# Optimization experiments

Hardware: AMD Instinct MI355X
Metric: run time of the kernel (lower is better)

The kernel has to match this reference:

```python
import jax, jax.numpy as jnp
import numpy as np

LABEL_SMOOTHING = 0.1
K_SLOPE = 5.0
N, D = 8192, 256


def setup_inputs() -> dict:
    key = jax.random.key(0)
    k1, k2, k3 = jax.random.split(key, 3)
    return {
        "image_features1": jax.random.normal(k1, (N, D), dtype=jnp.float32),
        "image_features2": jax.random.normal(k2, (N, D), dtype=jnp.float32),
        "logit_scale": jnp.asarray(14.2857, dtype=jnp.float32),  # ~ 1/0.07 CLIP temp
        "positive_weights": jax.random.normal(k3, (N,), dtype=jnp.float32),
    }


def _l2_normalize(x, axis=-1, eps=1e-12):
    # matches F.normalize(dim=-1)
    norm = jnp.linalg.norm(x, axis=axis, keepdims=True)
    return x / jnp.maximum(norm, eps)


def _weighted_infonce(sim, eps):
    # per row i: (1-eps_i)*(-sim[i,i] + lse_i) + eps_i*(-mean(sim[i,:]) + lse_i)
    #          = lse_i - (1-eps_i)*sim[i,i] - eps_i*mean_i
    n = sim.shape[0]
    lse = jax.nn.logsumexp(sim, axis=1)            # [n]
    diag = jnp.diagonal(sim)                       # [n]
    row_mean = jnp.mean(sim, axis=1)               # [n]
    per_row = lse - (1.0 - eps) * diag - eps * row_mean
    return jnp.sum(per_row) / n


def reference(image_features1, image_features2, logit_scale, positive_weights):
    f1 = _l2_normalize(image_features1)
    f2 = _l2_normalize(image_features2)
    logits12 = logit_scale * (f1 @ f2.T)           # [N, N]
    # eps = 1 - (1 - label_smoothing) * sigmoid(k * w)
    eps = 1.0 - (1.0 - LABEL_SMOOTHING) * jax.nn.sigmoid(K_SLOPE * positive_weights)
    loss1 = _weighted_infonce(logits12, eps)
    loss2 = _weighted_infonce(logits12.T, eps)
    return (loss1 + loss2) / 2.0
```

## Files before the change

kernel.cpp:

```cpp
#include <hip/hip_runtime.h>
#include <hip/hip_bf16.h>

#define NN 8192
#define DD 256
#define LOG2E 1.4426950408889634f
#define LN2f 0.6931471805599453f

typedef __attribute__((ext_vector_type(8))) short short8;
typedef __attribute__((ext_vector_type(4))) float f32x4;

__device__ __forceinline__ unsigned short f2bf(float x) {
    unsigned int u = __float_as_uint(x);
    u += 0x7fff + ((u >> 16) & 1);
    return (unsigned short)(u >> 16);
}
__device__ __forceinline__ float epsf(float w) {
    return 1.f - 0.9f / (1.f + __expf(-5.f * w));
}

__global__ __launch_bounds__(256) void nrm_kernel(
    const float* __restrict__ f1, const float* __restrict__ f2,
    const float* __restrict__ scale_p, const float* __restrict__ wts,
    unsigned short* __restrict__ f1n, unsigned short* __restrict__ f2n,
    float* __restrict__ diag, float* __restrict__ rse, float* __restrict__ cse,
    float* __restrict__ S1p, float* __restrict__ S2p,
    float* __restrict__ T1p, float* __restrict__ T2p)
{
    __shared__ float4 red[4][256];
    const int w = threadIdx.x >> 6, lane = threadIdx.x & 63;
    const int row = blockIdx.x * 4 + w;
    const float4 a = reinterpret_cast<const float4*>(f1 + (size_t)row * DD)[lane];
    const float4 b = reinterpret_cast<const float4*>(f2 + (size_t)row * DD)[lane];
    float sa = a.x * a.x + a.y * a.y + a.z * a.z + a.w * a.w;
    float sb = b.x * b.x + b.y * b.y + b.z * b.z + b.w * b.w;
    float sab = a.x * b.x + a.y * b.y + a.z * b.z + a.w * b.w;
#pragma unroll
    for (int off = 1; off < 64; off <<= 1) {
        sa += __shfl_xor(sa, off);
        sb += __shfl_xor(sb, off);
        sab += __shfl_xor(sab, off);
    }
    const float s = scale_p[0];
    const float n1 = fmaxf(sqrtf(sa), 1e-12f);
    const float n2 = fmaxf(sqrtf(sb), 1e-12f);
    const float e = epsf(wts[row]);
    if (lane == 0) { diag[row] = s * sab / (n1 * n2); rse[row] = 0.f; cse[row] = 0.f; }
    const float r1 = s * LOG2E / n1, r2 = 1.0f / n2;
    const float v0 = a.x * r1, v1 = a.y * r1, v2 = a.z * r1, v3 = a.w * r1;
    const float u0 = b.x * r2, u1 = b.y * r2, u2 = b.z * r2, u3 = b.w * r2;
    ushort4 o1, o2;
    o1.x = f2bf(v0); o1.y = f2bf(v1); o1.z = f2bf(v2); o1.w = f2bf(v3);
    o2.x = f2bf(u0); o2.y = f2bf(u1); o2.z = f2bf(u2); o2.w = f2bf(u3);
    reinterpret_cast<ushort4*>(f1n + (size_t)row * DD)[lane] = o1;
    reinterpret_cast<ushort4*>(f2n + (size_t)row * DD)[lane] = o2;
    red[w][lane * 4 + 0] = make_float4(v0, e * v0, u0, e * u0);
    red[w][lane * 4 + 1] = make_float4(v1, e * v1, u1, e * u1);
    red[w][lane * 4 + 2] = make_float4(v2, e * v2, u2, e * u2);
    red[w][lane * 4 + 3] = make_float4(v3, e * v3, u3, e * u3);
    __syncthreads();
    const int c = threadIdx.x;
    const int part = (blockIdx.x & 63) * 256 + c;
    const float4 q0 = red[0][c], q1 = red[1][c], q2 = red[2][c], q3 = red[3][c];
    atomicAdd(&S1p[part], q0.x + q1.x + q2.x + q3.x);
    atomicAdd(&T1p[part], q0.y + q1.y + q2.y + q3.y);
    atomicAdd(&S2p[part], q0.z + q1.z + q2.z + q3.z);
    atomicAdd(&T2p[part], q0.w + q1.w + q2.w + q3.w);
}

__global__ __launch_bounds__(256, 2) void gemm_kernel(
    const unsigned short* __restrict__ f1n, const unsigned short* __restrict__ f2n,
    float* __restrict__ rowsumexp, float* __restrict__ colsumexp)
{
    __shared__ char Bs[2][64 * 512];
    __shared__ float colbuf[2][1024];
    const int bid = blockIdx.x;
    const int bm = bid >> 3, bc = bid & 7;
    const int w = threadIdx.x >> 6, lane = threadIdx.x & 63;
    const int wr = (w >> 1) * 64, wc = (w & 1) * 32;
    const int lhi = lane >> 4, llo = lane & 15;

    const char* aBase = (const char*)f1n + ((size_t)(bm * 128 + wr + llo) * 512) + lhi * 16;
    short8 av[4][8];
#pragma unroll
    for (int m = 0; m < 4; ++m)
#pragma unroll
        for (int ks = 0; ks < 8; ++ks)
            av[m][ks] = *(const short8*)(aBase + (size_t)(m * 16) * 512 + ks * 64);
#pragma unroll
    for (int m = 0; m < 4; ++m)
#pragma unroll
        for (int ks = 0; ks < 8; ++ks)
            asm volatile("" : "+v"(av[m][ks]));

    const char* bBase = (const char*)f2n + (size_t)bc * 1024 * 512;

    auto stage = [&](int buf, int tile) {
#pragma unroll
        for (int i = 0; i < 8; ++i) {
            const int r = w * 16 + i * 2 + (lane >> 5);
            const int cs = (lane & 31) ^ (r & 15);
            __builtin_amdgcn_global_load_lds(
                (const __attribute__((address_space(1))) unsigned int*)
                    (bBase + (size_t)(tile * 64 + r) * 512 + cs * 16),
                (__attribute__((address_space(3))) unsigned int*)
                    (&Bs[buf][(w * 16 + i * 2) * 512]), 16, 0, 0);
        }
    };

    float rowpart[16];
#pragma unroll
    for (int i = 0; i < 16; ++i) rowpart[i] = 0.f;

    stage(0, 0);
    __syncthreads();

    const int rb0 = wc + llo, rb1 = wc + 16 + llo;
    const int sw = llo << 4;

    for (int t = 0; t < 16; ++t) {
        const int cur = t & 1;
        if (t < 15) stage(cur ^ 1, t + 1);

        f32x4 acc[4][2];
#pragma unroll
        for (int m = 0; m < 4; ++m) {
            acc[m][0] = (f32x4){0.f, 0.f, 0.f, 0.f};
            acc[m][1] = (f32x4){0.f, 0.f, 0.f, 0.f};
        }
        const char* bs = Bs[cur];
#pragma unroll
        for (int ks = 0; ks < 8; ++ks) {
            const int kb = ks * 64 + lhi * 16;
            const short8 bv0 = *(const short8*)(bs + rb0 * 512 + (kb ^ sw));
            const short8 bv1 = *(const short8*)(bs + rb1 * 512 + (kb ^ sw));
#pragma unroll
            for (int m = 0; m < 4; ++m) {
                acc[m][0] = __builtin_amdgcn_mfma_f32_16x16x32_bf16(av[m][ks], bv0, acc[m][0], 0, 0, 0);
                acc[m][1] = __builtin_amdgcn_mfma_f32_16x16x32_bf16(av[m][ks], bv1, acc[m][1], 0, 0, 0);
            }
        }

        float cee0 = 0.f, cee1 = 0.f;
#pragma unroll
        for (int m = 0; m < 4; ++m)
#pragma unroll
            for (int j = 0; j < 4; ++j) {
                const float e0 = __builtin_exp2f(acc[m][0][j]);
                const float e1 = __builtin_exp2f(acc[m][1][j]);
                rowpart[m * 4 + j] += e0 + e1;
                cee0 += e0; cee1 += e1;
            }
        cee0 += __shfl_xor(cee0, 16); cee0 += __shfl_xor(cee0, 32);
        cee1 += __shfl_xor(cee1, 16); cee1 += __shfl_xor(cee1, 32);
        if (lhi == 0) {
            colbuf[w >> 1][t * 64 + wc + llo] = cee0;
            colbuf[w >> 1][t * 64 + wc + 16 + llo] = cee1;
        }
        __syncthreads();
    }

#pragma unroll
    for (int m = 0; m < 4; ++m)
#pragma unroll
        for (int j = 0; j < 4; ++j) {
            float v = rowpart[m * 4 + j];
            v += __shfl_xor(v, 1); v += __shfl_xor(v, 2);
            v += __shfl_xor(v, 4); v += __shfl_xor(v, 8);
            if (llo == 0)
                atomicAdd(&rowsumexp[bm * 128 + wr + m * 16 + lhi * 4 + j], v);
        }
    for (int c = threadIdx.x; c < 1024; c += 256)
        atomicAdd(&colsumexp[bc * 1024 + c], colbuf[0][c] + colbuf[1][c]);
}

__global__ __launch_bounds__(1024) void fin_kernel(
    const float* __restrict__ rse, const float* __restrict__ cse,
    const float* __restrict__ diag, const float* __restrict__ wts,
    const float* __restrict__ S1p, const float* __restrict__ S2p,
    const float* __restrict__ T1p, const float* __restrict__ T2p,
    float* __restrict__ out)
{
    const int t = threadIdx.x;
    float a = 0.f;
#pragma unroll
    for (int k = 0; k < 8; ++k) {
        const int i = t + k * 1024;
        a += __logf(rse[i]) + __logf(cse[i]) - 2.f * (1.f - epsf(wts[i])) * diag[i];
    }
    __shared__ float4 pr4[4][256];
    {
        const int col = t & 255, seg = t >> 8;
        float s1 = 0.f, t1 = 0.f, s2 = 0.f, t2 = 0.f;
#pragma unroll
        for (int q = 0; q < 16; ++q) {
            const int idx = (seg * 16 + q) * 256 + col;
            s1 += S1p[idx]; t1 += T1p[idx]; s2 += S2p[idx]; t2 += T2p[idx];
        }
        pr4[seg][col] = make_float4(s1, t1, s2, t2);
    }
    __syncthreads();
    if (t < 256) {
        const float4 q0 = pr4[0][t], q1 = pr4[1][t], q2 = pr4[2][t], q3 = pr4[3][t];
        const float s1 = q0.x + q1.x + q2.x + q3.x;
        const float t1 = q0.y + q1.y + q2.y + q3.y;
        const float s2 = q0.z + q1.z + q2.z + q3.z;
        const float t2 = q0.w + q1.w + q2.w + q3.w;
        a -= (t1 * s2 + s1 * t2) * (LN2f / (float)NN);
    }
#pragma unroll
    for (int off = 1; off < 64; off <<= 1) a += __shfl_xor(a, off);
    __shared__ float red[16];
    if ((t & 63) == 0) red[t >> 6] = a;
    __syncthreads();
    if (t == 0) {
        float tot = 0.f;
#pragma unroll
        for (int i = 0; i < 16; ++i) tot += red[i];
        out[0] = tot * (1.f / (2.f * (float)NN));
    }
}

extern "C" void kernel_launch(void* const* d_in, const int* in_sizes, int n_in,
                              void* d_out, int out_size, void* d_ws, size_t ws_size,
                              hipStream_t stream) {
    (void)in_sizes; (void)n_in; (void)out_size; (void)ws_size;
    const float* f1 = (const float*)d_in[0];
    const float* f2 = (const float*)d_in[1];
    const float* scale = (const float*)d_in[2];
    const float* wts = (const float*)d_in[3];
    float* out = (float*)d_out;

    char* ws = (char*)d_ws;
    unsigned short* f1n = (unsigned short*)ws;
    unsigned short* f2n = (unsigned short*)(ws + (size_t)4 * 1024 * 1024);
    float* fb = (float*)(ws + (size_t)8 * 1024 * 1024);
    float* rse  = fb;
    float* cse  = fb + 8192;
    float* diag = fb + 16384;
    float* S1p  = fb + 24576;
    float* S2p  = fb + 24576 + 16384;
    float* T1p  = fb + 24576 + 32768;
    float* T2p  = fb + 24576 + 49152;

    hipMemsetAsync(S1p, 0, (size_t)4 * 16384 * sizeof(float), stream);
    nrm_kernel<<<NN / 4, 256, 0, stream>>>(f1, f2, scale, wts, f1n, f2n,
                                           diag, rse, cse, S1p, S2p, T1p, T2p);
    gemm_kernel<<<512, 256, 0, stream>>>(f1n, f2n, rse, cse);
    fin_kernel<<<1, 1024, 0, stream>>>(rse, cse, diag, wts, S1p, S2p, T1p, T2p, out);
}
```

Before: 77.67 us.

## Shrink GEMM tiles to 64x512 with 2048 blocks and split final reduction

The GEMM block tile drops from 128x1024 to 64x512 rows/cols, giving 2048 blocks instead of 512. Each wave now does 2 MFMAs per k-step instead of 8, with half the LDS and occupancy raised to 4 blocks per CU. The single-block final kernel is split into a 32-block log/diag reduction with an atomic total and a second kernel for the dot-product correction, adding an extra launch. Smaller tiles halve the A-fragment and B reuse per block, so global and LDS traffic per FLOP rises, and the row/col atomics increase fourfold.

```diff
diff --git a/kernel.cpp b/kernel.cpp
--- a/kernel.cpp
+++ b/kernel.cpp
@@ -67,126 +67,124 @@
     atomicAdd(&T2p[part], q0.w + q1.w + q2.w + q3.w);
 }
 
-__global__ __launch_bounds__(256, 2) void gemm_kernel(
+__global__ __launch_bounds__(256, 4) void gemm_kernel(
     const unsigned short* __restrict__ f1n, const unsigned short* __restrict__ f2n,
     float* __restrict__ rowsumexp, float* __restrict__ colsumexp)
 {
-    __shared__ char Bs[2][64 * 512];
-    __shared__ float colbuf[2][1024];
+    __shared__ char Bs[2][32 * 512];
+    __shared__ float colbuf[2][512];
     const int bid = blockIdx.x;
-    const int bm = bid >> 3, bc = bid & 7;
+    const int bm = bid >> 4, bc = bid & 15;
     const int w = threadIdx.x >> 6, lane = threadIdx.x & 63;
-    const int wr = (w >> 1) * 64, wc = (w & 1) * 32;
+    const int wq = w >> 1;
+    const int wc2 = w & 1;
     const int lhi = lane >> 4, llo = lane & 15;
 
-    const char* aBase = (const char*)f1n + ((size_t)(bm * 128 + wr + llo) * 512) + lhi * 16;
-    short8 av[4][8];
-#pragma unroll
-    for (int m = 0; m < 4; ++m)
+    const char* aBase = (const char*)f1n + ((size_t)(bm * 64 + wq * 32 + llo) * 512) + lhi * 16;
+    short8 av[2][8];
+#pragma unroll
+    for (int m = 0; m < 2; ++m)
 #pragma unroll
         for (int ks = 0; ks < 8; ++ks)
             av[m][ks] = *(const short8*)(aBase + (size_t)(m * 16) * 512 + ks * 64);
 #pragma unroll
-    for (int m = 0; m < 4; ++m)
+    for (int m = 0; m < 2; ++m)
 #pragma unroll
         for (int ks = 0; ks < 8; ++ks)
             asm volatile("" : "+v"(av[m][ks]));
 
-    const char* bBase = (const char*)f2n + (size_t)bc * 1024 * 512;
+    const char* bBase = (const char*)f2n + (size_t)bc * 512 * 512;
 
     auto stage = [&](int buf, int tile) {
 #pragma unroll
-        for (int i = 0; i < 8; ++i) {
-            const int r = w * 16 + i * 2 + (lane >> 5);
+        for (int i = 0; i < 4; ++i) {
+            const int r = w * 8 + i * 2 + (lane >> 5);
             const int cs = (lane & 31) ^ (r & 15);
             __builtin_amdgcn_global_load_lds(
                 (const __attribute__((address_space(1))) unsigned int*)
-                    (bBase + (size_t)(tile * 64 + r) * 512 + cs * 16),
+                    (bBase + (size_t)(tile * 32 + r) * 512 + cs * 16),
                 (__attribute__((address_space(3))) unsigned int*)
-                    (&Bs[buf][(w * 16 + i * 2) * 512]), 16, 0, 0);
+                    (&Bs[buf][(w * 8 + i * 2) * 512]), 16, 0, 0);
         }
     };
 
-    float rowpart[16];
-#pragma unroll
-    for (int i = 0; i < 16; ++i) rowpart[i] = 0.f;
+    float rowpart[8];
+#pragma unroll
+    for (int i = 0; i < 8; ++i) rowpart[i] = 0.f;
 
     stage(0, 0);
     __syncthreads();
 
-    const int rb0 = wc + llo, rb1 = wc + 16 + llo;
+    const int rb = wc2 * 16 + llo;
     const int sw = llo << 4;
 
     for (int t = 0; t < 16; ++t) {
         const int cur = t & 1;
         if (t < 15) stage(cur ^ 1, t + 1);
 
-        f32x4 acc[4][2];
-#pragma unroll
-        for (int m = 0; m < 4; ++m) {
-            acc[m][0] = (f32x4){0.f, 0.f, 0.f, 0.f};
-            acc[m][1] = (f32x4){0.f, 0.f, 0.f, 0.f};
-        }
+        f32x4 acc[2];
+        acc[0] = (f32x4){0.f, 0.f, 0.f, 0.f};
+        acc[1] = (f32x4){0.f, 0.f, 0.f, 0.f};
         const char* bs = Bs[cur];
 #pragma unroll
         for (int ks = 0; ks < 8; ++ks) {
             const int kb = ks * 64 + lhi * 16;
-            const short8 bv0 = *(const short8*)(bs + rb0 * 512 + (kb ^ sw));
-            const short8 bv1 = *(const short8*)(bs + rb1 * 512 + (kb ^ sw));
-#pragma unroll
-            for (int m = 0; m < 4; ++m) {
-                acc[m][0] = __builtin_amdgcn_mfma_f32_16x16x32_bf16(av[m][ks], bv0, acc[m][0], 0, 0, 0);
-                acc[m][1] = __builtin_amdgcn_mfma_f32_16x16x32_bf16(av[m][ks], bv1, acc[m][1], 0, 0, 0);
+            const short8 bv = *(const short8*)(bs + rb * 512 + (kb ^ sw));
+            acc[0] = __builtin_amdgcn_mfma_f32_16x16x32_bf16(av[0][ks], bv, acc[0], 0, 0, 0);
+            acc[1] = __builtin_amdgcn_mfma_f32_16x16x32_bf16(av[1][ks], bv, acc[1], 0, 0, 0);
+        }
+
+        float cee = 0.f;
+#pragma unroll
+        for (int m = 0; m < 2; ++m)
+#pragma unroll
+            for (int j = 0; j < 4; ++j) {
+                const float e = __builtin_exp2f(acc[m][j]);
+                rowpart[m * 4 + j] += e;
+                cee += e;
             }
-        }
-
-        float cee0 = 0.f, cee1 = 0.f;
-#pragma unroll
-        for (int m = 0; m < 4; ++m)
-#pragma unroll
-            for (int j = 0; j < 4; ++j) {
-                const float e0 = __builtin_exp2f(acc[m][0][j]);
-                const float e1 = __builtin_exp2f(acc[m][1][j]);
-                rowpart[m * 4 + j] += e0 + e1;
-                cee0 += e0; cee1 += e1;
-            }
-        cee0 += __shfl_xor(cee0, 16); cee0 += __shfl_xor(cee0, 32);
-        cee1 += __shfl_xor(cee1, 16); cee1 += __shfl_xor(cee1, 32);
-        if (lhi == 0) {
-            colbuf[w >> 1][t * 64 + wc + llo] = cee0;
-            colbuf[w >> 1][t * 64 + wc + 16 + llo] = cee1;
-        }
+        cee += __shfl_xor(cee, 16); cee += __shfl_xor(cee, 32);
+        if (lhi == 0) colbuf[wq][t * 32 + wc2 * 16 + llo] = cee;
         __syncthreads();
     }
 
 #pragma unroll
-    for (int m = 0; m < 4; ++m)
+    for (int m = 0; m < 2; ++m)
 #pragma unroll
         for (int j = 0; j < 4; ++j) {
             float v = rowpart[m * 4 + j];
             v += __shfl_xor(v, 1); v += __shfl_xor(v, 2);
             v += __shfl_xor(v, 4); v += __shfl_xor(v, 8);
             if (llo == 0)
-                atomicAdd(&rowsumexp[bm * 128 + wr + m * 16 + lhi * 4 + j], v);
-        }
-    for (int c = threadIdx.x; c < 1024; c += 256)
-        atomicAdd(&colsumexp[bc * 1024 + c], colbuf[0][c] + colbuf[1][c]);
-}
-
-__global__ __launch_bounds__(1024) void fin_kernel(
+                atomicAdd(&rowsumexp[bm * 64 + wq * 32 + m * 16 + lhi * 4 + j], v);
+        }
+    for (int c = threadIdx.x; c < 512; c += 256)
+        atomicAdd(&colsumexp[bc * 512 + c], colbuf[0][c] + colbuf[1][c]);
+}
+
+__global__ __launch_bounds__(256) void finA_kernel(
     const float* __restrict__ rse, const float* __restrict__ cse,
     const float* __restrict__ diag, const float* __restrict__ wts,
+    float* __restrict__ totalp)
+{
+    const int i = blockIdx.x * 256 + threadIdx.x;
+    const float eps = epsf(wts[i]);
+    float a = __logf(rse[i]) + __logf(cse[i]) - 2.f * (1.f - eps) * diag[i];
+#pragma unroll
+    for (int off = 1; off < 64; off <<= 1) a += __shfl_xor(a, off);
+    __shared__ float red[4];
+    if ((threadIdx.x & 63) == 0) red[threadIdx.x >> 6] = a;
+    __syncthreads();
+    if (threadIdx.x == 0)
+        atomicAdd(totalp, red[0] + red[1] + red[2] + red[3]);
+}
+
+__global__ __launch_bounds__(1024) void finB_kernel(
     const float* __restrict__ S1p, const float* __restrict__ S2p,
     const float* __restrict__ T1p, const float* __restrict__ T2p,
-    float* __restrict__ out)
+    const float* __restrict__ totalp, float* __restrict__ out)
 {
     const int t = threadIdx.x;
-    float a = 0.f;
-#pragma unroll
-    for (int k = 0; k < 8; ++k) {
-        const int i = t + k * 1024;
-        a += __logf(rse[i]) + __logf(cse[i]) - 2.f * (1.f - epsf(wts[i])) * diag[i];
-    }
     __shared__ float4 pr4[4][256];
     {
         const int col = t & 255, seg = t >> 8;
@@ -199,13 +197,14 @@
         pr4[seg][col] = make_float4(s1, t1, s2, t2);
     }
     __syncthreads();
+    float a = 0.f;
     if (t < 256) {
         const float4 q0 = pr4[0][t], q1 = pr4[1][t], q2 = pr4[2][t], q3 = pr4[3][t];
         const float s1 = q0.x + q1.x + q2.x + q3.x;
         const float t1 = q0.y + q1.y + q2.y + q3.y;
         const float s2 = q0.z + q1.z + q2.z + q3.z;
         const float t2 = q0.w + q1.w + q2.w + q3.w;
-        a -= (t1 * s2 + s1 * t2) * (LN2f / (float)NN);
+        a = (t1 * s2 + s1 * t2) * (LN2f / (float)NN);
     }
 #pragma unroll
     for (int off = 1; off < 64; off <<= 1) a += __shfl_xor(a, off);
@@ -213,10 +212,10 @@
     if ((t & 63) == 0) red[t >> 6] = a;
     __syncthreads();
     if (t == 0) {
-        float tot = 0.f;
-#pragma unroll
-        for (int i = 0; i < 16; ++i) tot += red[i];
-        out[0] = tot * (1.f / (2.f * (float)NN));
+        float dot = 0.f;
+#pragma unroll
+        for (int i = 0; i < 16; ++i) dot += red[i];
+        out[0] = (totalp[0] - dot) * (1.f / (2.f * (float)NN));
     }
 }
 
@@ -241,10 +240,12 @@
     float* S2p  = fb + 24576 + 16384;
     float* T1p  = fb + 24576 + 32768;
     float* T2p  = fb + 24576 + 49152;
-
-    hipMemsetAsync(S1p, 0, (size_t)4 * 16384 * sizeof(float), stream);
+    float* totalp = fb + 24576 + 65536;
+
+    hipMemsetAsync(S1p, 0, ((size_t)4 * 16384 + 16) * sizeof(float), stream);
     nrm_kernel<<<NN / 4, 256, 0, stream>>>(f1, f2, scale, wts, f1n, f2n,
                                            diag, rse, cse, S1p, S2p, T1p, T2p);
-    gemm_kernel<<<512, 256, 0, stream>>>(f1n, f2n, rse, cse);
-    fin_kernel<<<1, 1024, 0, stream>>>(rse, cse, diag, wts, S1p, S2p, T1p, T2p, out);
-}
+    gemm_kernel<<<2048, 256, 0, stream>>>(f1n, f2n, rse, cse);
+    finA_kernel<<<32, 256, 0, stream>>>(rse, cse, diag, wts, totalp);
+    finB_kernel<<<1, 1024, 0, stream>>>(S1p, S2p, T1p, T2p, totalp, out);
+}
```

Result: slower. 140.8 us (+81.2%).
